# Performance work log

Hardware: AMD Instinct MI355X
Metric: run time of the kernel (lower is better)

## Reference

```python
import jax, jax.numpy as jnp
import numpy as np

K = 5        # pooling kernel size (k_size)
DILATE = 2   # unfold dilation
PAD = (K // 2) * DILATE


def setup_inputs() -> dict:
    key = jax.random.key(0)
    kx, km = jax.random.split(key)
    b, c, h, w = 8, 64, 256, 256
    x = jax.random.normal(kx, (b, c, h, w), dtype=jnp.float32)
    mask = jax.random.randint(km, (b, 1, h, w), 0, 4).astype(jnp.float32)
    return {"x": x, "mask": mask}


def reference(x, mask):
    # x: (b,c,h,w), mask: (b,1,h,w).
    # Equivalent to: reflect-pad, unfold into k^2 windows, keep window taps whose
    # mask value equals the center mask value, mean over the kept taps.
    b, c, h, w = x.shape
    pad_cfg = ((0, 0), (0, 0), (PAD, PAD), (PAD, PAD))
    xp = jnp.pad(x, pad_cfg, mode="reflect")      # (b,c,h+2P,w+2P)
    mp = jnp.pad(mask, pad_cfg, mode="reflect")   # (b,1,h+2P,w+2P)

    acc = jnp.zeros_like(x)                       # sum of matched neighbor values
    cnt = jnp.zeros((b, 1, h, w), dtype=x.dtype)  # number of matched taps per pixel
    for i in range(K):           # small fixed k^2 loop; each iter is fused elementwise
        oi = i * DILATE
        for j in range(K):
            oj = j * DILATE
            xw = jax.lax.dynamic_slice(xp, (0, 0, oi, oj), (b, c, h, w))
            mw = jax.lax.dynamic_slice(mp, (0, 0, oi, oj), (b, 1, h, w))
            match = (mw == mask).astype(x.dtype)  # (b,1,h,w)
            acc = acc + match * xw
            cnt = cnt + match

    denom = jnp.where(cnt == 0, jnp.ones_like(cnt), cnt)
    return acc / denom
```

## Files before the change

kernel.cpp:

```cpp
#include <hip/hip_runtime.h>
#include <cstdint>


#define B_ 8
#define C_ 64
#define H_ 256
#define W_ 256
#define NHW (H_ * W_)

__device__ __forceinline__ int reflect_i(int v, int n) {
  v = v < 0 ? -v : v;
  return v >= n ? 2 * n - 2 - v : v;
}

__global__ __launch_bounds__(256, 4)
void selected_meanpool_kernel(const float* __restrict__ x,
                              const float* __restrict__ mask,
                              float* __restrict__ out) {
  __shared__ float smem[4][5][264];

  const int bid  = blockIdx.x;
  const int b    = bid & 7;
  const int h    = bid >> 3;
  const int tid  = threadIdx.x;
  const int wv   = tid >> 6;
  const int lane = tid & 63;
  const int w0   = lane << 2;

  int hre[5];
#pragma unroll
  for (int r = 0; r < 5; ++r) hre[r] = reflect_i(h + 2 * r - 4, H_);

  const float* mb = mask + b * NHW;
  float mc[4];
#pragma unroll
  for (int p = 0; p < 4; ++p) mc[p] = mb[h * W_ + w0 + p];

  int wre[4][5];
#pragma unroll
  for (int p = 0; p < 4; ++p)
#pragma unroll
    for (int jc = 0; jc < 5; ++jc)
      wre[p][jc] = reflect_i(w0 + p + 2 * jc - 4, W_);

  uint32_t bits[4] = {0u, 0u, 0u, 0u};
#pragma unroll
  for (int r = 0; r < 5; ++r) {
    const float* mrow = mb + hre[r] * W_;
#pragma unroll
    for (int jc = 0; jc < 5; ++jc) {
#pragma unroll
      for (int p = 0; p < 4; ++p) {
        float mv = mrow[wre[p][jc]];
        if (mv == mc[p]) bits[p] |= (1u << (r * 5 + jc));
      }
    }
  }
  float inv[4];
#pragma unroll
  for (int p = 0; p < 4; ++p) inv[p] = 1.0f / (float)__builtin_popcount(bits[p]);

  const float* xb = x + (size_t)b * C_ * NHW;
  float*       ob = out + (size_t)b * C_ * NHW;

  for (int g = 0; g < 16; ++g) {
#pragma unroll
    for (int k = 0; k < 5; ++k) {
      int pair = 4 * k + wv;
      int cl = pair / 5, r = pair % 5;
      const float* src = xb + (4 * g + cl) * NHW + hre[r] * W_ + (lane << 2);
      float4 v = *(const float4*)src;
      *(float4*)&smem[cl][r][4 + (lane << 2)] = v;
    }
    if (tid < 160) {
      int hp = tid >> 3, l3 = tid & 7;
      int cl = hp / 5, r = hp % 5;
      const float* rowp = xb + (4 * g + cl) * NHW + hre[r] * W_;
      if (l3 < 4) smem[cl][r][l3]       = rowp[4 - l3];
      else        smem[cl][r][256 + l3] = rowp[258 - l3];
    }
    __syncthreads();

    float acc[4] = {0.f, 0.f, 0.f, 0.f};
#pragma unroll
    for (int r = 0; r < 5; ++r) {
      float4 f0 = *(const float4*)&smem[wv][r][w0];
      float4 f1 = *(const float4*)&smem[wv][r][w0 + 4];
      float4 f2 = *(const float4*)&smem[wv][r][w0 + 8];
      float win[12] = {f0.x, f0.y, f0.z, f0.w,
                       f1.x, f1.y, f1.z, f1.w,
                       f2.x, f2.y, f2.z, f2.w};
#pragma unroll
      for (int jc = 0; jc < 5; ++jc) {
        const int t = r * 5 + jc;
#pragma unroll
        for (int p = 0; p < 4; ++p) {
#if __has_builtin(__builtin_amdgcn_sbfe)
          int m = __builtin_amdgcn_sbfe((int)bits[p], t, 1);
#else
          int m = ((int)(bits[p] << (31 - t))) >> 31;
#endif
          acc[p] += __int_as_float(__float_as_int(win[p + 2 * jc]) & m);
        }
      }
    }
    float4 o;
    o.x = acc[0] * inv[0];
    o.y = acc[1] * inv[1];
    o.z = acc[2] * inv[2];
    o.w = acc[3] * inv[3];
    *(float4*)&ob[(4 * g + wv) * NHW + h * W_ + w0] = o;
    __syncthreads();
  }
}

extern "C" void kernel_launch(void* const* d_in, const int* in_sizes, int n_in,
                              void* d_out, int out_size, void* d_ws, size_t ws_size,
                              hipStream_t stream) {
  const float* x    = (const float*)d_in[0];
  const float* mask = (const float*)d_in[1];
  float*       out  = (float*)d_out;
  dim3 grid(B_ * H_);
  dim3 block(256);
  hipLaunchKernelGGL(selected_meanpool_kernel, grid, block, 0, stream,
                     x, mask, out);
}
```

Baseline: 301.2 us.

## Drop shared-memory staging; load halo windows directly from global with register prefetch

Removes the LDS tile and both per-iteration block barriers. Each wave now loads its own channel's 5 rows straight from global memory as three overlapping float4 loads per row, fixing up the reflect padding at the edges in registers. The next row's loads are prefetched while the current row is accumulated. The mask window is built the same way with vector loads, and occupancy is raised to 8 blocks per CU. In exchange, global/L2 traffic goes up because each input row is read three times, and register pressure is higher.

```diff
diff --git a/kernel.cpp b/kernel.cpp
--- a/kernel.cpp
+++ b/kernel.cpp
@@ -13,12 +13,10 @@
   return v >= n ? 2 * n - 2 - v : v;
 }
 
-__global__ __launch_bounds__(256, 4)
+__global__ __launch_bounds__(256, 8)
 void selected_meanpool_kernel(const float* __restrict__ x,
                               const float* __restrict__ mask,
                               float* __restrict__ out) {
-  __shared__ float smem[4][5][264];
-
   const int bid  = blockIdx.x;
   const int b    = bid & 7;
   const int h    = bid >> 3;
@@ -32,29 +30,26 @@
   for (int r = 0; r < 5; ++r) hre[r] = reflect_i(h + 2 * r - 4, H_);
 
   const float* mb = mask + b * NHW;
-  float mc[4];
-#pragma unroll
-  for (int p = 0; p < 4; ++p) mc[p] = mb[h * W_ + w0 + p];
-
-  int wre[4][5];
-#pragma unroll
-  for (int p = 0; p < 4; ++p)
-#pragma unroll
-    for (int jc = 0; jc < 5; ++jc)
-      wre[p][jc] = reflect_i(w0 + p + 2 * jc - 4, W_);
+  float4 mc4 = *(const float4*)&mb[h * W_ + w0];
+  float mcv[4] = {mc4.x, mc4.y, mc4.z, mc4.w};
 
   uint32_t bits[4] = {0u, 0u, 0u, 0u};
 #pragma unroll
   for (int r = 0; r < 5; ++r) {
     const float* mrow = mb + hre[r] * W_;
+    float4 f0 = *(const float4*)&mrow[lane == 0 ? 0 : w0 - 4];
+    float4 f1 = *(const float4*)&mrow[w0];
+    float4 f2 = *(const float4*)&mrow[lane == 63 ? 252 : w0 + 4];
+    if (lane == 0)  { f0.x = f2.x; f0.y = f1.w; f0.z = f1.z; f0.w = f1.y; }
+    if (lane == 63) { f2.x = f1.z; f2.y = f1.y; f2.z = f1.x; f2.w = f0.w; }
+    float win[12] = {f0.x, f0.y, f0.z, f0.w,
+                     f1.x, f1.y, f1.z, f1.w,
+                     f2.x, f2.y, f2.z, f2.w};
 #pragma unroll
-    for (int jc = 0; jc < 5; ++jc) {
+    for (int jc = 0; jc < 5; ++jc)
 #pragma unroll
-      for (int p = 0; p < 4; ++p) {
-        float mv = mrow[wre[p][jc]];
-        if (mv == mc[p]) bits[p] |= (1u << (r * 5 + jc));
-      }
-    }
+      for (int p = 0; p < 4; ++p)
+        if (win[p + 2 * jc] == mcv[p]) bits[p] |= (1u << (r * 5 + jc));
   }
   float inv[4];
 #pragma unroll
@@ -63,30 +58,26 @@
   const float* xb = x + (size_t)b * C_ * NHW;
   float*       ob = out + (size_t)b * C_ * NHW;
 
-  for (int g = 0; g < 16; ++g) {
-#pragma unroll
-    for (int k = 0; k < 5; ++k) {
-      int pair = 4 * k + wv;
-      int cl = pair / 5, r = pair % 5;
-      const float* src = xb + (4 * g + cl) * NHW + hre[r] * W_ + (lane << 2);
-      float4 v = *(const float4*)src;
-      *(float4*)&smem[cl][r][4 + (lane << 2)] = v;
-    }
-    if (tid < 160) {
-      int hp = tid >> 3, l3 = tid & 7;
-      int cl = hp / 5, r = hp % 5;
-      const float* rowp = xb + (4 * g + cl) * NHW + hre[r] * W_;
-      if (l3 < 4) smem[cl][r][l3]       = rowp[4 - l3];
-      else        smem[cl][r][256 + l3] = rowp[258 - l3];
-    }
-    __syncthreads();
+  for (int ci = 0; ci < 16; ++ci) {
+    const int c = 4 * ci + wv;
+    const float* xc = xb + (size_t)c * NHW;
+    float acc[4] = {0.f, 0.f, 0.f, 0.f};
 
-    float acc[4] = {0.f, 0.f, 0.f, 0.f};
+    const float* row0 = xc + hre[0] * W_;
+    float4 f0 = *(const float4*)&row0[lane == 0 ? 0 : w0 - 4];
+    float4 f1 = *(const float4*)&row0[w0];
+    float4 f2 = *(const float4*)&row0[lane == 63 ? 252 : w0 + 4];
 #pragma unroll
     for (int r = 0; r < 5; ++r) {
-      float4 f0 = *(const float4*)&smem[wv][r][w0];
-      float4 f1 = *(const float4*)&smem[wv][r][w0 + 4];
-      float4 f2 = *(const float4*)&smem[wv][r][w0 + 8];
+      float4 g0, g1, g2;
+      if (r < 4) {
+        const float* nrow = xc + hre[r + 1] * W_;
+        g0 = *(const float4*)&nrow[lane == 0 ? 0 : w0 - 4];
+        g1 = *(const float4*)&nrow[w0];
+        g2 = *(const float4*)&nrow[lane == 63 ? 252 : w0 + 4];
+      }
+      if (lane == 0)  { f0.x = f2.x; f0.y = f1.w; f0.z = f1.z; f0.w = f1.y; }
+      if (lane == 63) { f2.x = f1.z; f2.y = f1.y; f2.z = f1.x; f2.w = f0.w; }
       float win[12] = {f0.x, f0.y, f0.z, f0.w,
                        f1.x, f1.y, f1.z, f1.w,
                        f2.x, f2.y, f2.z, f2.w};
@@ -103,14 +94,14 @@
           acc[p] += __int_as_float(__float_as_int(win[p + 2 * jc]) & m);
         }
       }
+      if (r < 4) { f0 = g0; f1 = g1; f2 = g2; }
     }
     float4 o;
     o.x = acc[0] * inv[0];
     o.y = acc[1] * inv[1];
     o.z = acc[2] * inv[2];
     o.w = acc[3] * inv[3];
-    *(float4*)&ob[(4 * g + wv) * NHW + h * W_ + w0] = o;
-    __syncthreads();
+    *(float4*)&ob[(size_t)c * NHW + h * W_ + w0] = o;
   }
 }
 
```

After: 417.3 us. +38.5%, slower.
